# Performance work log

Measured on AMD Instinct MI355X. Metric: run time of the kernel, lower is better.

## Reference

```python
import jax, jax.numpy as jnp
import numpy as np

B, L, D, H = 4, 2048, 1024, 16
DH = D // H

def setup_inputs() -> dict:
    key = jax.random.key(0)
    k1, k2, k3 = jax.random.split(key, 3)
    x = jax.random.normal(k1, (B, L, D), dtype=jnp.float32)
    w_qkv = jax.random.normal(k2, (3 * D, D), dtype=jnp.float32) * (1.0 / np.sqrt(D))
    w_proj = jax.random.normal(k3, (D, D), dtype=jnp.float32) * (1.0 / np.sqrt(D))
    return {"x": x, "w_qkv": w_qkv, "w_proj": w_proj}

def reference(x, w_qkv, w_proj):
    b, l, d = x.shape
    scale = 1.0 / np.sqrt(DH)
    qkv = (x @ w_qkv.T).reshape(b, l, 3, H, DH)
    qkv = jnp.transpose(qkv, (2, 0, 3, 1, 4))
    q, k, v = qkv[0], qkv[1], qkv[2]
    scores = jnp.einsum('bhqd,bhkd->bhqk', q, k) * scale
    attn = jax.nn.softmax(scores, axis=-1)
    out = jnp.einsum('bhqk,bhkd->bhqd', attn, v)
    out = jnp.transpose(out, (0, 2, 1, 3)).reshape(b, l, d)
    return out @ w_proj.T
```

## Files before the change

### kernel.cpp

```cpp
#include <hip/hip_runtime.h>
#include <hip/hip_bf16.h>


typedef __bf16  bf16x8  __attribute__((ext_vector_type(8)));
typedef __bf16  bf16x4  __attribute__((ext_vector_type(4)));
typedef float   floatx4 __attribute__((ext_vector_type(4)));

__device__ __forceinline__ void async_ld16(const void* g, void* lds_base_uniform) {
  __builtin_amdgcn_global_load_lds(
      (const __attribute__((address_space(1))) void*)g,
      (__attribute__((address_space(3))) void*)lds_base_uniform,
      16, 0, 0);
}

__device__ __forceinline__ int detect_bf16(const void* p) {
  const unsigned short* u = (const unsigned short*)p;
  int sane = 0;
#pragma unroll 4
  for (int i = 0; i < 64; ++i) {
    unsigned short w = u[2 * i];
    int e = (w >> 7) & 0xFF;
    sane += (w == 0 || (e >= 100 && e <= 150)) ? 1 : 0;
  }
  return sane >= 32;
}

__device__ __forceinline__ bf16x8 ld8_f32cvt(const void* base, size_t elem) {
  const float* p = (const float*)base + elem;
  floatx4 u0 = *(const floatx4*)p;
  floatx4 u1 = *(const floatx4*)(p + 4);
  bf16x8 v;
  v[0] = (__bf16)u0[0]; v[1] = (__bf16)u0[1]; v[2] = (__bf16)u0[2]; v[3] = (__bf16)u0[3];
  v[4] = (__bf16)u1[0]; v[5] = (__bf16)u1[1]; v[6] = (__bf16)u1[2]; v[7] = (__bf16)u1[3];
  return v;
}

template<int CTRL>
__device__ __forceinline__ float dpp_f(float x) {
  return __builtin_bit_cast(float,
      __builtin_amdgcn_update_dpp(0, __builtin_bit_cast(int, x), CTRL, 0xF, 0xF, true));
}
__device__ __forceinline__ float row16_sum(float x) {
  x += dpp_f<0xB1>(x);
  x += dpp_f<0x4E>(x);
  x += dpp_f<0x141>(x);
  x += dpp_f<0x140>(x);
  return x;
}

__launch_bounds__(256)
__global__ void cvt3_kernel(const void* __restrict__ s0, __bf16* __restrict__ d0, int n0,
                            const void* __restrict__ s1, __bf16* __restrict__ d1, int n1,
                            const void* __restrict__ s2, __bf16* __restrict__ d2) {
  int u = blockIdx.x * blockDim.x + threadIdx.x;
  const void* src; __bf16* dst;
  if (u < n0)           { src = s0; dst = d0; }
  else if (u < n0 + n1) { src = s1; dst = d1; u -= n0; }
  else                  { src = s2; dst = d2; u -= n0 + n1; }
  const int lane = threadIdx.x & 63;
  int det = (lane == 0) ? detect_bf16(src) : 0;
  const int is_bf16 = __builtin_amdgcn_readfirstlane(det);
  const size_t e = (size_t)u * 8;
  if (is_bf16) *(bf16x8*)(dst + e) = *(const bf16x8*)((const __bf16*)src + e);
  else         *(bf16x8*)(dst + e) = ld8_f32cvt(src, e);
}

template<int EPI>
__launch_bounds__(256, 2)
__global__ void gemm_bt_kernel(const __bf16* __restrict__ A,
                               const __bf16* __restrict__ B,
                               const void* __restrict__ oprobe,
                               void* __restrict__ Cout,
                               __bf16* __restrict__ qkb,
                               __bf16* __restrict__ vtb,
                               int M, int N, int K)
{
  __shared__ __align__(16) __bf16 SM[9216];
  __bf16* As = SM;
  __bf16* Bs = SM + 4096;

  const int flat = blockIdx.x;
  const int m0 = (((flat & 7) << 3) | ((flat >> 3) & 7)) << 7;
  const int n0 = (flat >> 6) << 7;

  const int tid  = threadIdx.x;
  const int wave = tid >> 6;
  const int lane = tid & 63;
  const int quad = lane >> 4;
  const int l16  = lane & 15;
  const int wm   = wave >> 1;
  const int wn   = wave & 1;

  const int r_in   = lane >> 2;
  const int cchunk = lane & 3;

  const __bf16* Ab = A + (size_t)m0 * K;
  const __bf16* Bb = B + (size_t)n0 * K;

  floatx4 acc[4][4];
#pragma unroll
  for (int i = 0; i < 4; ++i)
#pragma unroll
    for (int j = 0; j < 4; ++j)
      acc[i][j] = (floatx4){0.f, 0.f, 0.f, 0.f};

  const int ca0 = wave * 2;
  for (int k0 = 0; k0 < K; k0 += 32) {
#pragma unroll
    for (int i = 0; i < 2; ++i) {
      const int ca  = ca0 + i;
      const int row = ca * 16 + r_in;
      async_ld16(Ab + (size_t)row * K + k0 + cchunk * 8, (char*)As + ca * 1024);
      async_ld16(Bb + (size_t)row * K + k0 + cchunk * 8, (char*)Bs + ca * 1024);
    }
    __syncthreads();

    bf16x8 af[4], bfr[4];
#pragma unroll
    for (int tt = 0; tt < 4; ++tt) {
      af[tt]  = *(const bf16x8*)&As[(wm * 64 + tt * 16 + l16) * 32 + quad * 8];
      bfr[tt] = *(const bf16x8*)&Bs[(wn * 64 + tt * 16 + l16) * 32 + quad * 8];
    }
#pragma unroll
    for (int mt = 0; mt < 4; ++mt)
#pragma unroll
      for (int nt = 0; nt < 4; ++nt)
        acc[mt][nt] = __builtin_amdgcn_mfma_f32_16x16x32_bf16(af[mt], bfr[nt], acc[mt][nt], 0, 0, 0);
    __syncthreads();
  }

  if (EPI == 1) {
    const int out_bf16 = detect_bf16(oprobe);
#pragma unroll
    for (int mt = 0; mt < 4; ++mt) {
#pragma unroll
      for (int nt = 0; nt < 4; ++nt) {
        const int n_idx = n0 + wn * 64 + nt * 16 + l16;
        const int mbase = m0 + wm * 64 + mt * 16 + quad * 4;
        if (out_bf16) {
#pragma unroll
          for (int r = 0; r < 4; ++r)
            ((__bf16*)Cout)[(size_t)(mbase + r) * N + n_idx] = (__bf16)acc[mt][nt][r];
        } else {
#pragma unroll
          for (int r = 0; r < 4; ++r)
            ((float*)Cout)[(size_t)(mbase + r) * N + n_idx] = acc[mt][nt][r];
        }
      }
    }
  } else {
    const int sel = n0 >> 10;
    if (sel < 2) {
      __bf16* eQ = SM + wave * (16 * 72);
      const int ncol = n0 + wn * 64;
      const int mb   = m0 + wm * 64;
      const int rl   = lane >> 3;
      const int ch   = lane & 7;
#pragma unroll
      for (int mt = 0; mt < 4; ++mt) {
#pragma unroll
        for (int nt = 0; nt < 4; ++nt)
#pragma unroll
          for (int r = 0; r < 4; ++r)
            eQ[(quad * 4 + r) * 72 + nt * 16 + l16] = (__bf16)acc[mt][nt][r];
        __builtin_amdgcn_wave_barrier();
#pragma unroll
        for (int i = 0; i < 2; ++i) {
          const int row = rl + 8 * i;
          bf16x8 v = *(const bf16x8*)&eQ[row * 72 + ch * 8];
          const size_t m = (size_t)(mb + mt * 16 + row);
          *(bf16x8*)&qkb[m * 2048 + ncol + ch * 8] = v;
        }
        __builtin_amdgcn_wave_barrier();
      }
    } else {
#pragma unroll
      for (int mt = 0; mt < 4; ++mt) {
#pragma unroll
        for (int nt = 0; nt < 4; ++nt) {
          const int n_idx = n0 + wn * 64 + nt * 16 + l16;
          const int mbase = m0 + wm * 64 + mt * 16 + quad * 4;
          const int rem = n_idx & 1023;
          const int h   = rem >> 6;
          const int dh  = rem & 63;
          const int b   = mbase >> 11;
          const int l   = mbase & 2047;
          const int bh  = b * 16 + h;
          bf16x4 pk;
#pragma unroll
          for (int r = 0; r < 4; ++r) pk[r] = (__bf16)acc[mt][nt][r];
          *(bf16x4*)&vtb[((size_t)bh * 64 + dh) * 2048 + l] = pk;
        }
      }
    }
  }
}

__launch_bounds__(256, 4)
__global__ void attn_kernel(const __bf16* __restrict__ qkb,
                            const __bf16* __restrict__ vtb,
                            __bf16* __restrict__ ob )
{
  __shared__ __align__(16) __bf16 S[2][2 * 64 * 72];

  const int tid  = threadIdx.x;
  const int wave = tid >> 6;
  const int lane = tid & 63;
  const int quad = lane >> 4;
  const int l16  = lane & 15;

  const int bh = blockIdx.y;
  const int b  = bh >> 4;
  const int h  = bh & 15;
  const int q0 = blockIdx.x * 128;

  const __bf16* Qp = qkb + (size_t)b * 2048 * 2048 + h * 64;
  const __bf16* Kp = Qp + 1024;
  const __bf16* Vp = vtb + (size_t)bh * 64 * 2048;

  const float C1 = 0.125f * 1.44269504f;
  const float C2 = -8.0f  * 1.44269504f;

  bf16x8 aq[2][2];
#pragma unroll
  for (int rt = 0; rt < 2; ++rt) {
    const __bf16* qrow = Qp + (size_t)(q0 + wave * 32 + rt * 16 + l16) * 2048;
    aq[rt][0] = *(const bf16x8*)(qrow + quad * 8);
    aq[rt][1] = *(const bf16x8*)(qrow + 32 + quad * 8);
  }

  bf16x8 onesb;
  {
    const __bf16 ov = (l16 == 0) ? (__bf16)1.0f : (__bf16)0.0f;
#pragma unroll
    for (int i = 0; i < 8; ++i) onesb[i] = ov;
  }

  floatx4 o[2][4], o5[2];
#pragma unroll
  for (int rt = 0; rt < 2; ++rt) {
    o5[rt] = (floatx4){0.f, 0.f, 0.f, 0.f};
#pragma unroll
    for (int dt = 0; dt < 4; ++dt) o[rt][dt] = (floatx4){0.f, 0.f, 0.f, 0.f};
  }

  const int sarr = wave >> 1;
  const int srb  = (wave & 1) * 32;
  const int sr0  = lane >> 3;
  const int scol = (lane & 7) * 8;

  {
    __bf16* dst = &S[0][sarr * (64 * 72)];
    if (sarr == 0) {
#pragma unroll
      for (int i = 0; i < 4; ++i) {
        const int row = srb + sr0 + 8 * i;
        *(bf16x8*)&dst[row * 72 + scol] = *(const bf16x8*)(Kp + (size_t)row * 2048 + scol);
      }
    } else {
#pragma unroll
      for (int i = 0; i < 4; ++i) {
        const int row = srb + sr0 + 8 * i;
        *(bf16x8*)&dst[row * 72 + scol] = *(const bf16x8*)(Vp + (size_t)row * 2048 + scol);
      }
    }
  }
  __syncthreads();

  for (int kt = 0; kt < 32; ++kt) {
    const int cur = kt & 1;
    const int nxt = cur ^ 1;
    const int kn  = (((kt + 1) & 31) << 6);

    bf16x8 sreg[4];
    if (sarr == 0) {
#pragma unroll
      for (int i = 0; i < 4; ++i) {
        const int row = srb + sr0 + 8 * i;
        sreg[i] = *(const bf16x8*)(Kp + (size_t)(kn + row) * 2048 + scol);
      }
    } else {
#pragma unroll
      for (int i = 0; i < 4; ++i) {
        const int row = srb + sr0 + 8 * i;
        sreg[i] = *(const bf16x8*)(Vp + (size_t)row * 2048 + kn + scol);
      }
    }

    const __bf16* Kc = &S[cur][0];
    const __bf16* Vc = &S[cur][64 * 72];
    __bf16*       Pq = &S[nxt][0] + wave * 2304;

    floatx4 st[2][4];
    __builtin_amdgcn_s_setprio(1);
#pragma unroll
    for (int nt = 0; nt < 4; ++nt) {
      const int krow = nt * 16 + l16;
      bf16x8 ak0 = *(const bf16x8*)&Kc[krow * 72 + quad * 8];
      bf16x8 ak1 = *(const bf16x8*)&Kc[krow * 72 + 32 + quad * 8];
#pragma unroll
      for (int rt = 0; rt < 2; ++rt) {
        floatx4 z = (floatx4){0.f, 0.f, 0.f, 0.f};
        z = __builtin_amdgcn_mfma_f32_16x16x32_bf16(ak0, aq[rt][0], z, 0, 0, 0);
        z = __builtin_amdgcn_mfma_f32_16x16x32_bf16(ak1, aq[rt][1], z, 0, 0, 0);
        st[rt][nt] = z;
      }
    }
    __builtin_amdgcn_s_setprio(0);

#pragma unroll
    for (int rt = 0; rt < 2; ++rt) {
#pragma unroll
      for (int nt = 0; nt < 4; ++nt) {
        bf16x4 pk;
#pragma unroll
        for (int r = 0; r < 4; ++r)
          pk[r] = (__bf16)__builtin_amdgcn_exp2f(fmaf(st[rt][nt][r], C1, C2));
        *(bf16x4*)&Pq[(rt * 16 + l16) * 72 + nt * 16 + quad * 4] = pk;
      }
    }

    __builtin_amdgcn_wave_barrier();

    bf16x8 ap[2][2];
#pragma unroll
    for (int rt = 0; rt < 2; ++rt) {
      ap[rt][0] = *(const bf16x8*)&Pq[(rt * 16 + l16) * 72 + quad * 8];
      ap[rt][1] = *(const bf16x8*)&Pq[(rt * 16 + l16) * 72 + 32 + quad * 8];
    }

    __builtin_amdgcn_s_setprio(1);
#pragma unroll
    for (int dt = 0; dt < 4; ++dt) {
      const int vrow = dt * 16 + l16;
      bf16x8 bv0 = *(const bf16x8*)&Vc[vrow * 72 + quad * 8];
      bf16x8 bv1 = *(const bf16x8*)&Vc[vrow * 72 + 32 + quad * 8];
#pragma unroll
      for (int rt = 0; rt < 2; ++rt) {
        o[rt][dt] = __builtin_amdgcn_mfma_f32_16x16x32_bf16(ap[rt][0], bv0, o[rt][dt], 0, 0, 0);
        o[rt][dt] = __builtin_amdgcn_mfma_f32_16x16x32_bf16(ap[rt][1], bv1, o[rt][dt], 0, 0, 0);
      }
    }
#pragma unroll
    for (int rt = 0; rt < 2; ++rt) {
      o5[rt] = __builtin_amdgcn_mfma_f32_16x16x32_bf16(ap[rt][0], onesb, o5[rt], 0, 0, 0);
      o5[rt] = __builtin_amdgcn_mfma_f32_16x16x32_bf16(ap[rt][1], onesb, o5[rt], 0, 0, 0);
    }
    __builtin_amdgcn_s_setprio(0);

    __builtin_amdgcn_wave_barrier();

    {
      __bf16* dst = &S[nxt][sarr * (64 * 72)];
#pragma unroll
      for (int i = 0; i < 4; ++i) {
        const int row = srb + sr0 + 8 * i;
        *(bf16x8*)&dst[row * 72 + scol] = sreg[i];
      }
    }
    __syncthreads();
  }

#pragma unroll
  for (int rt = 0; rt < 2; ++rt)
#pragma unroll
    for (int r = 0; r < 4; ++r) {
      const float lv  = row16_sum(l16 == 0 ? o5[rt][r] : 0.f);
      const float inv = 1.f / lv;
      const size_t rowbase =
          ((size_t)b * 2048 + q0 + wave * 32 + rt * 16 + quad * 4 + r) * 1024 + h * 64;
#pragma unroll
      for (int dt = 0; dt < 4; ++dt)
        ob[rowbase + dt * 16 + l16] = (__bf16)(o[rt][dt][r] * inv);
    }
}

extern "C" void kernel_launch(void* const* d_in, const int* in_sizes, int n_in,
                              void* d_out, int out_size, void* d_ws, size_t ws_size,
                              hipStream_t stream)
{
  (void)in_sizes; (void)n_in; (void)out_size; (void)ws_size;

  const void* x     = d_in[0];
  const void* wqkv  = d_in[1];
  const void* wproj = d_in[2];

  const size_t NX    = (size_t)8192 * 1024;
  const size_t NWQKV = (size_t)3072 * 1024;
  const size_t NWPRJ = (size_t)1024 * 1024;

  __bf16* qkbuf  = (__bf16*)d_ws;
  __bf16* vtbuf  = qkbuf + 2 * NX;
  __bf16* abuf   = vtbuf + NX;
  __bf16* xb     = abuf + NX;
  __bf16* wqkvb  = xb + NX;
  __bf16* wprojb = wqkvb + NWQKV;

  dim3 blk(256);

  cvt3_kernel<<<dim3((NX + NWQKV + NWPRJ) / 2048), blk, 0, stream>>>(
      x, xb, NX / 8, wqkv, wqkvb, NWQKV / 8, wproj, wprojb);

  gemm_bt_kernel<0><<<dim3(24 * 64), blk, 0, stream>>>(
      xb, wqkvb, nullptr, nullptr, qkbuf, vtbuf, 8192, 3072, 1024);

  attn_kernel<<<dim3(2048 / 128, 64), blk, 0, stream>>>(qkbuf, vtbuf, abuf);

  gemm_bt_kernel<1><<<dim3(8 * 64), blk, 0, stream>>>(
      abuf, wprojb, wproj, d_out, nullptr, nullptr, 8192, 1024, 1024);
}
```

Baseline: 285.3 us.

## Use two-wave attention blocks with 64 query rows per wave

Attention blocks now run 128 threads (2 waves) instead of 4. Each wave handles 64 query rows instead of 32, so every K/V fragment read from LDS feeds twice as many MFMAs. Wave 0 stages K and wave 1 stages V, each loading a full 64-row tile. The cost is more registers for accumulators and Q/P fragments, fewer waves per block to hide latency, and each wave's P scratch doubling in size. The EPI=1 GEMM epilogue now also runs bf16 detection on lane 0 only and broadcasts it, instead of every lane running it.

After: 286.3 us. Within noise of the previous version (+0.4%).

```diff
diff --git a/kernel.cpp b/kernel.cpp
--- a/kernel.cpp
+++ b/kernel.cpp
@@ -23,6 +23,12 @@
     sane += (w == 0 || (e >= 100 && e <= 150)) ? 1 : 0;
   }
   return sane >= 32;
+}
+
+__device__ __forceinline__ int detect_bf16_wave(const void* p) {
+  const int lane = threadIdx.x & 63;
+  int det = (lane == 0) ? detect_bf16(p) : 0;
+  return __builtin_amdgcn_readfirstlane(det);
 }
 
 __device__ __forceinline__ bf16x8 ld8_f32cvt(const void* base, size_t elem) {
@@ -57,9 +63,7 @@
   if (u < n0)           { src = s0; dst = d0; }
   else if (u < n0 + n1) { src = s1; dst = d1; u -= n0; }
   else                  { src = s2; dst = d2; u -= n0 + n1; }
-  const int lane = threadIdx.x & 63;
-  int det = (lane == 0) ? detect_bf16(src) : 0;
-  const int is_bf16 = __builtin_amdgcn_readfirstlane(det);
+  const int is_bf16 = detect_bf16_wave(src);
   const size_t e = (size_t)u * 8;
   if (is_bf16) *(bf16x8*)(dst + e) = *(const bf16x8*)((const __bf16*)src + e);
   else         *(bf16x8*)(dst + e) = ld8_f32cvt(src, e);
@@ -130,7 +134,7 @@
   }
 
   if (EPI == 1) {
-    const int out_bf16 = detect_bf16(oprobe);
+    const int out_bf16 = detect_bf16_wave(oprobe);
 #pragma unroll
     for (int mt = 0; mt < 4; ++mt) {
 #pragma unroll
@@ -196,7 +200,7 @@
   }
 }
 
-__launch_bounds__(256, 4)
+__launch_bounds__(128, 2)
 __global__ void attn_kernel(const __bf16* __restrict__ qkb,
                             const __bf16* __restrict__ vtb,
                             __bf16* __restrict__ ob )
@@ -221,10 +225,10 @@
   const float C1 = 0.125f * 1.44269504f;
   const float C2 = -8.0f  * 1.44269504f;
 
-  bf16x8 aq[2][2];
-#pragma unroll
-  for (int rt = 0; rt < 2; ++rt) {
-    const __bf16* qrow = Qp + (size_t)(q0 + wave * 32 + rt * 16 + l16) * 2048;
+  bf16x8 aq[4][2];
+#pragma unroll
+  for (int rt = 0; rt < 4; ++rt) {
+    const __bf16* qrow = Qp + (size_t)(q0 + wave * 64 + rt * 16 + l16) * 2048;
     aq[rt][0] = *(const bf16x8*)(qrow + quad * 8);
     aq[rt][1] = *(const bf16x8*)(qrow + 32 + quad * 8);
   }
@@ -236,33 +240,24 @@
     for (int i = 0; i < 8; ++i) onesb[i] = ov;
   }
 
-  floatx4 o[2][4], o5[2];
-#pragma unroll
-  for (int rt = 0; rt < 2; ++rt) {
+  floatx4 o[4][4], o5[4];
+#pragma unroll
+  for (int rt = 0; rt < 4; ++rt) {
     o5[rt] = (floatx4){0.f, 0.f, 0.f, 0.f};
 #pragma unroll
     for (int dt = 0; dt < 4; ++dt) o[rt][dt] = (floatx4){0.f, 0.f, 0.f, 0.f};
   }
 
-  const int sarr = wave >> 1;
-  const int srb  = (wave & 1) * 32;
   const int sr0  = lane >> 3;
   const int scol = (lane & 7) * 8;
+  const __bf16* Sp = (wave == 0) ? Kp : Vp;
 
   {
-    __bf16* dst = &S[0][sarr * (64 * 72)];
-    if (sarr == 0) {
-#pragma unroll
-      for (int i = 0; i < 4; ++i) {
-        const int row = srb + sr0 + 8 * i;
-        *(bf16x8*)&dst[row * 72 + scol] = *(const bf16x8*)(Kp + (size_t)row * 2048 + scol);
-      }
-    } else {
-#pragma unroll
-      for (int i = 0; i < 4; ++i) {
-        const int row = srb + sr0 + 8 * i;
-        *(bf16x8*)&dst[row * 72 + scol] = *(const bf16x8*)(Vp + (size_t)row * 2048 + scol);
-      }
+    __bf16* dst = &S[0][wave * 4608];
+#pragma unroll
+    for (int i = 0; i < 8; ++i) {
+      const int row = sr0 + 8 * i;
+      *(bf16x8*)&dst[row * 72 + scol] = *(const bf16x8*)(Sp + (size_t)row * 2048 + scol);
     }
   }
   __syncthreads();
@@ -272,59 +267,54 @@
     const int nxt = cur ^ 1;
     const int kn  = (((kt + 1) & 31) << 6);
 
-    bf16x8 sreg[4];
-    if (sarr == 0) {
-#pragma unroll
-      for (int i = 0; i < 4; ++i) {
-        const int row = srb + sr0 + 8 * i;
-        sreg[i] = *(const bf16x8*)(Kp + (size_t)(kn + row) * 2048 + scol);
-      }
-    } else {
-#pragma unroll
-      for (int i = 0; i < 4; ++i) {
-        const int row = srb + sr0 + 8 * i;
-        sreg[i] = *(const bf16x8*)(Vp + (size_t)row * 2048 + kn + scol);
-      }
+    bf16x8 sreg[8];
+#pragma unroll
+    for (int i = 0; i < 8; ++i) {
+      const int row = sr0 + 8 * i;
+      sreg[i] = (wave == 0)
+          ? *(const bf16x8*)(Sp + (size_t)(kn + row) * 2048 + scol)
+          : *(const bf16x8*)(Sp + (size_t)row * 2048 + kn + scol);
     }
 
     const __bf16* Kc = &S[cur][0];
-    const __bf16* Vc = &S[cur][64 * 72];
-    __bf16*       Pq = &S[nxt][0] + wave * 2304;
-
-    floatx4 st[2][4];
-    __builtin_amdgcn_s_setprio(1);
+    const __bf16* Vc = &S[cur][4608];
+    __bf16*       Pq = &S[nxt][wave * 4608];
+
+    bf16x8 ak[4][2];
 #pragma unroll
     for (int nt = 0; nt < 4; ++nt) {
       const int krow = nt * 16 + l16;
-      bf16x8 ak0 = *(const bf16x8*)&Kc[krow * 72 + quad * 8];
-      bf16x8 ak1 = *(const bf16x8*)&Kc[krow * 72 + 32 + quad * 8];
-#pragma unroll
-      for (int rt = 0; rt < 2; ++rt) {
+      ak[nt][0] = *(const bf16x8*)&Kc[krow * 72 + quad * 8];
+      ak[nt][1] = *(const bf16x8*)&Kc[krow * 72 + 32 + quad * 8];
+    }
+
+#pragma unroll
+    for (int rt = 0; rt < 4; ++rt) {
+      floatx4 st[4];
+      __builtin_amdgcn_s_setprio(1);
+#pragma unroll
+      for (int nt = 0; nt < 4; ++nt) {
         floatx4 z = (floatx4){0.f, 0.f, 0.f, 0.f};
-        z = __builtin_amdgcn_mfma_f32_16x16x32_bf16(ak0, aq[rt][0], z, 0, 0, 0);
-        z = __builtin_amdgcn_mfma_f32_16x16x32_bf16(ak1, aq[rt][1], z, 0, 0, 0);
-        st[rt][nt] = z;
-      }
-    }
-    __builtin_amdgcn_s_setprio(0);
-
-#pragma unroll
-    for (int rt = 0; rt < 2; ++rt) {
+        z = __builtin_amdgcn_mfma_f32_16x16x32_bf16(ak[nt][0], aq[rt][0], z, 0, 0, 0);
+        z = __builtin_amdgcn_mfma_f32_16x16x32_bf16(ak[nt][1], aq[rt][1], z, 0, 0, 0);
+        st[nt] = z;
+      }
+      __builtin_amdgcn_s_setprio(0);
 #pragma unroll
       for (int nt = 0; nt < 4; ++nt) {
         bf16x4 pk;
 #pragma unroll
         for (int r = 0; r < 4; ++r)
-          pk[r] = (__bf16)__builtin_amdgcn_exp2f(fmaf(st[rt][nt][r], C1, C2));
+          pk[r] = (__bf16)__builtin_amdgcn_exp2f(fmaf(st[nt][r], C1, C2));
         *(bf16x4*)&Pq[(rt * 16 + l16) * 72 + nt * 16 + quad * 4] = pk;
       }
     }
 
     __builtin_amdgcn_wave_barrier();
 
-    bf16x8 ap[2][2];
-#pragma unroll
-    for (int rt = 0; rt < 2; ++rt) {
+    bf16x8 ap[4][2];
+#pragma unroll
+    for (int rt = 0; rt < 4; ++rt) {
       ap[rt][0] = *(const bf16x8*)&Pq[(rt * 16 + l16) * 72 + quad * 8];
       ap[rt][1] = *(const bf16x8*)&Pq[(rt * 16 + l16) * 72 + 32 + quad * 8];
     }
@@ -336,13 +326,13 @@
       bf16x8 bv0 = *(const bf16x8*)&Vc[vrow * 72 + quad * 8];
       bf16x8 bv1 = *(const bf16x8*)&Vc[vrow * 72 + 32 + quad * 8];
 #pragma unroll
-      for (int rt = 0; rt < 2; ++rt) {
+      for (int rt = 0; rt < 4; ++rt) {
         o[rt][dt] = __builtin_amdgcn_mfma_f32_16x16x32_bf16(ap[rt][0], bv0, o[rt][dt], 0, 0, 0);
         o[rt][dt] = __builtin_amdgcn_mfma_f32_16x16x32_bf16(ap[rt][1], bv1, o[rt][dt], 0, 0, 0);
       }
     }
 #pragma unroll
-    for (int rt = 0; rt < 2; ++rt) {
+    for (int rt = 0; rt < 4; ++rt) {
       o5[rt] = __builtin_amdgcn_mfma_f32_16x16x32_bf16(ap[rt][0], onesb, o5[rt], 0, 0, 0);
       o5[rt] = __builtin_amdgcn_mfma_f32_16x16x32_bf16(ap[rt][1], onesb, o5[rt], 0, 0, 0);
     }
@@ -351,10 +341,10 @@
     __builtin_amdgcn_wave_barrier();
 
     {
-      __bf16* dst = &S[nxt][sarr * (64 * 72)];
-#pragma unroll
-      for (int i = 0; i < 4; ++i) {
-        const int row = srb + sr0 + 8 * i;
+      __bf16* dst = &S[nxt][wave * 4608];
+#pragma unroll
+      for (int i = 0; i < 8; ++i) {
+        const int row = sr0 + 8 * i;
         *(bf16x8*)&dst[row * 72 + scol] = sreg[i];
       }
     }
@@ -362,13 +352,13 @@
   }
 
 #pragma unroll
-  for (int rt = 0; rt < 2; ++rt)
+  for (int rt = 0; rt < 4; ++rt)
 #pragma unroll
     for (int r = 0; r < 4; ++r) {
       const float lv  = row16_sum(l16 == 0 ? o5[rt][r] : 0.f);
       const float inv = 1.f / lv;
       const size_t rowbase =
-          ((size_t)b * 2048 + q0 + wave * 32 + rt * 16 + quad * 4 + r) * 1024 + h * 64;
+          ((size_t)b * 2048 + q0 + wave * 64 + rt * 16 + quad * 4 + r) * 1024 + h * 64;
 #pragma unroll
       for (int dt = 0; dt < 4; ++dt)
         ob[rowbase + dt * 16 + l16] = (__bf16)(o[rt][dt][r] * inv);
@@ -396,16 +386,14 @@
   __bf16* wqkvb  = xb + NX;
   __bf16* wprojb = wqkvb + NWQKV;
 
-  dim3 blk(256);
-
-  cvt3_kernel<<<dim3((NX + NWQKV + NWPRJ) / 2048), blk, 0, stream>>>(
+  cvt3_kernel<<<dim3((NX + NWQKV + NWPRJ) / 2048), dim3(256), 0, stream>>>(
       x, xb, NX / 8, wqkv, wqkvb, NWQKV / 8, wproj, wprojb);
 
-  gemm_bt_kernel<0><<<dim3(24 * 64), blk, 0, stream>>>(
+  gemm_bt_kernel<0><<<dim3(24 * 64), dim3(256), 0, stream>>>(
       xb, wqkvb, nullptr, nullptr, qkbuf, vtbuf, 8192, 3072, 1024);
 
-  attn_kernel<<<dim3(2048 / 128, 64), blk, 0, stream>>>(qkbuf, vtbuf, abuf);
-
-  gemm_bt_kernel<1><<<dim3(8 * 64), blk, 0, stream>>>(
+  attn_kernel<<<dim3(2048 / 128, 64), dim3(128), 0, stream>>>(qkbuf, vtbuf, abuf);
+
+  gemm_bt_kernel<1><<<dim3(8 * 64), dim3(256), 0, stream>>>(
       abuf, wprojb, wproj, d_out, nullptr, nullptr, 8192, 1024, 1024);
 }
```
